# Performance work log

Measured on AMD Instinct MI355X. Metric: run time of the kernel, lower is better.

The kernel has to match this reference:

```python
import jax, jax.numpy as jnp
import numpy as np
from jax import lax

B, C, H, W = 4, 64, 128, 128
G, K, RED = 16, 7, 4        # groups, kernel size, reduce ratio
CR = C // RED               # reduced channels for kernel generation
EPS = 1e-5                  # BatchNorm eps (torch default)
DN = ('NCHW', 'OIHW', 'NCHW')


def setup_inputs() -> dict:
    key = jax.random.key(0)
    ks = jax.random.split(key, 5)
    return {
        'input': jax.random.normal(ks[0], (B, C, H, W), jnp.float32),
        # initial_mapping: depthwise 3x3 conv + pointwise 1x1 conv (bias=False)
        'w_dw': jax.random.normal(ks[1], (C, 1, 3, 3), jnp.float32) * 0.1,
        'w_pw': jax.random.normal(ks[2], (C, C), jnp.float32) * (1.0 / np.sqrt(C)),
        # sigma_mapping BatchNorm affine params
        'bn_gamma': jnp.ones((CR,), jnp.float32),
        'bn_beta': jnp.zeros((CR,), jnp.float32),
        # reduce / span 1x1 convs (bias=False)
        'w_reduce': jax.random.normal(ks[3], (CR, C), jnp.float32) * (1.0 / np.sqrt(C)),
        'w_span': jax.random.normal(ks[4], (K * K * G, CR), jnp.float32) * (1.0 / np.sqrt(CR)),
    }


def reference(input, w_dw, w_pw, bn_gamma, bn_beta, w_reduce, w_span):
    x = input
    # initial mapping: depthwise 3x3 (pad 1) then 1x1 pointwise
    h = lax.conv_general_dilated(x, w_dw, (1, 1), [(1, 1), (1, 1)],
                                 feature_group_count=C, dimension_numbers=DN)
    h = jnp.einsum('bchw,oc->bohw', h, w_pw)
    # unfold -> [B, C*K*K, H, W] with channel-major feature ordering (matches torch Unfold)
    patches = lax.conv_general_dilated_patches(h, (K, K), (1, 1), [(3, 3), (3, 3)],
                                               dimension_numbers=DN)
    patches = patches.reshape(B, G, C // G, K * K, H, W)
    # kernel generation: o_mapping is identity (stride 1 avg pool), then reduce -> BN(train) -> ReLU -> span
    r = jnp.einsum('bchw,oc->bohw', x, w_reduce)           # [B, CR, H, W]
    mean = r.mean(axis=(0, 2, 3), keepdims=True)
    var = r.var(axis=(0, 2, 3), keepdims=True)             # biased var, as torch BN training
    r = (r - mean) * lax.rsqrt(var + EPS) * bn_gamma[None, :, None, None] + bn_beta[None, :, None, None]
    r = jax.nn.relu(r)
    kern = jnp.einsum('bchw,oc->bohw', r, w_span)          # [B, G*K*K, H, W]
    kern = kern.reshape(B, G, 1, K * K, H, W)
    out = (kern * patches).sum(axis=3)                     # [B, G, C//G, H, W]
    return out.reshape(B, C, H, W)
```

## Files before the change

### kernel.cpp

```cpp
#include <hip/hip_runtime.h>

typedef _Float16 half2v __attribute__((ext_vector_type(2)));
typedef _Float16 half4v __attribute__((ext_vector_type(4)));
typedef _Float16 half8v __attribute__((ext_vector_type(8)));
typedef float f32x4 __attribute__((ext_vector_type(4)));

__launch_bounds__(256, 4)
__global__ void k_front(const float* __restrict__ in, const float* __restrict__ wdw,
                        const float* __restrict__ wpw, const float* __restrict__ wred,
                        _Float16* __restrict__ h16, _Float16* __restrict__ r16,
                        float* __restrict__ partial){
  __shared__ float4 s_in4[4][10][12];
  __shared__ __attribute__((aligned(16))) _Float16 s_dwh[64][72];
  __shared__ __attribute__((aligned(16))) _Float16 s_cvh[64][72];
  __shared__ float s_red[4][32];
  int t = threadIdx.x;
  int w = t >> 6, lane = t & 63;
  int lx = lane & 7, ly = lane >> 3;
  int c15 = lane & 15, hi = lane >> 4;
  int blk0 = blockIdx.x;

  int blk = ((blk0 & 7) << 7) | (blk0 >> 3);
  int tile = blk & 255, b = blk >> 8;
  int x0 = (tile & 15) << 3, y0 = (tile >> 4) << 3;
  const float* inb = in + ((long)b << 20) + ((long)(w << 2) << 14);

  const float* ap = wpw + (((w << 4) + c15) << 6) + (hi << 3);
  float4 ap0 = *(const float4*)(ap);
  float4 ap1 = *(const float4*)(ap + 4);
  float4 ap2 = *(const float4*)(ap + 32);
  float4 ap3 = *(const float4*)(ap + 36);
  const float* arp = wred + (c15 << 6) + (hi << 3);
  float4 ar0 = *(const float4*)(arp);
  float4 ar1 = *(const float4*)(arp + 4);
  float4 ar2 = *(const float4*)(arp + 32);
  float4 ar3 = *(const float4*)(arp + 36);
  half8v a_pw0 = {(_Float16)ap0.x,(_Float16)ap0.y,(_Float16)ap0.z,(_Float16)ap0.w,
                  (_Float16)ap1.x,(_Float16)ap1.y,(_Float16)ap1.z,(_Float16)ap1.w};
  half8v a_pw1 = {(_Float16)ap2.x,(_Float16)ap2.y,(_Float16)ap2.z,(_Float16)ap2.w,
                  (_Float16)ap3.x,(_Float16)ap3.y,(_Float16)ap3.z,(_Float16)ap3.w};
  half8v a_rd0 = {(_Float16)ar0.x,(_Float16)ar0.y,(_Float16)ar0.z,(_Float16)ar0.w,
                  (_Float16)ar1.x,(_Float16)ar1.y,(_Float16)ar1.z,(_Float16)ar1.w};
  half8v a_rd1 = {(_Float16)ar2.x,(_Float16)ar2.y,(_Float16)ar2.z,(_Float16)ar2.w,
                  (_Float16)ar3.x,(_Float16)ar3.y,(_Float16)ar3.z,(_Float16)ar3.w};

  int p1 = lane + 64;
  int ry0 = lane / 10, rx0 = lane - ry0 * 10;
  int ry1 = p1 / 10,   rx1 = p1 - ry1 * 10;
  int yy0 = y0 + ry0 - 1, xx0 = x0 + rx0 - 1;
  int yy1 = y0 + ry1 - 1, xx1 = x0 + rx1 - 1;
  bool ok0 = (unsigned)yy0 < 128u && (unsigned)xx0 < 128u;
  bool ok1 = (p1 < 100) && ((unsigned)yy1 < 128u) && ((unsigned)xx1 < 128u);
  int o0 = (yy0 << 7) + xx0, o1 = (yy1 << 7) + xx1;

  auto dw_dep = [&](int q){
    int wdbase = __builtin_amdgcn_readfirstlane(((q << 4) + (w << 2)) * 9);
    const float* wd = wdw + wdbase;
    float4 a = make_float4(0.f,0.f,0.f,0.f);
    float4 cv = make_float4(0.f,0.f,0.f,0.f);
    #pragma unroll
    for (int dy = 0; dy < 3; dy++){
      #pragma unroll
      for (int dx = 0; dx < 3; dx++){
        float4 v = s_in4[w][ly + dy][lx + dx];
        int k = dy * 3 + dx;
        a.x += v.x * wd[k];
        a.y += v.y * wd[9 + k];
        a.z += v.z * wd[18 + k];
        a.w += v.w * wd[27 + k];
        if (k == 4) cv = v;
      }
    }
    int cb = (q << 4) + (w << 2);
    half4v ah = {(_Float16)a.x,(_Float16)a.y,(_Float16)a.z,(_Float16)a.w};
    half4v eh = {(_Float16)cv.x,(_Float16)cv.y,(_Float16)cv.z,(_Float16)cv.w};
    *(half4v*)&s_dwh[lane][cb] = ah;
    *(half4v*)&s_cvh[lane][cb] = eh;
  };

  float4 vA0 = make_float4(0.f,0.f,0.f,0.f), vA1 = vA0, vB0 = vA0, vB1 = vA0;
  if (ok0){ vA0.x = inb[o0]; vA0.y = inb[o0+16384]; vA0.z = inb[o0+32768]; vA0.w = inb[o0+49152]; }
  if (ok1){ vA1.x = inb[o1]; vA1.y = inb[o1+16384]; vA1.z = inb[o1+32768]; vA1.w = inb[o1+49152]; }
  {
    const float* p1q = inb + (1L << 18);
    if (ok0){ vB0.x = p1q[o0]; vB0.y = p1q[o0+16384]; vB0.z = p1q[o0+32768]; vB0.w = p1q[o0+49152]; }
    if (ok1){ vB1.x = p1q[o1]; vB1.y = p1q[o1+16384]; vB1.z = p1q[o1+32768]; vB1.w = p1q[o1+49152]; }
  }

  #pragma unroll
  for (int qq = 0; qq < 2; qq++){
    s_in4[w][ry0][rx0] = vA0;
    if (p1 < 100) s_in4[w][ry1][rx1] = vA1;
    __builtin_amdgcn_wave_barrier();
    if (qq == 0){
      const float* pq = inb + (2L << 18);
      vA0 = make_float4(0.f,0.f,0.f,0.f); vA1 = vA0;
      if (ok0){ vA0.x = pq[o0]; vA0.y = pq[o0+16384]; vA0.z = pq[o0+32768]; vA0.w = pq[o0+49152]; }
      if (ok1){ vA1.x = pq[o1]; vA1.y = pq[o1+16384]; vA1.z = pq[o1+32768]; vA1.w = pq[o1+49152]; }
    }
    dw_dep(qq << 1);
    __builtin_amdgcn_wave_barrier();

    s_in4[w][ry0][rx0] = vB0;
    if (p1 < 100) s_in4[w][ry1][rx1] = vB1;
    __builtin_amdgcn_wave_barrier();
    if (qq == 0){
      const float* pq = inb + (3L << 18);
      vB0 = make_float4(0.f,0.f,0.f,0.f); vB1 = vB0;
      if (ok0){ vB0.x = pq[o0]; vB0.y = pq[o0+16384]; vB0.z = pq[o0+32768]; vB0.w = pq[o0+49152]; }
      if (ok1){ vB1.x = pq[o1]; vB1.y = pq[o1+16384]; vB1.z = pq[o1+32768]; vB1.w = pq[o1+49152]; }
    }
    dw_dep((qq << 1) + 1);
    __builtin_amdgcn_wave_barrier();
  }

  __syncthreads();

  f32x4 z = {0.f,0.f,0.f,0.f};
  f32x4 acc[4] = {z, z, z, z};
  #pragma unroll
  for (int tt = 0; tt < 4; tt++){
    half8v b0 = *(const half8v*)&s_dwh[(tt << 4) + c15][hi << 3];
    half8v b1 = *(const half8v*)&s_dwh[(tt << 4) + c15][32 + (hi << 3)];
    acc[tt] = __builtin_amdgcn_mfma_f32_16x16x32_f16(a_pw0, b0, acc[tt], 0, 0, 0);
    acc[tt] = __builtin_amdgcn_mfma_f32_16x16x32_f16(a_pw1, b1, acc[tt], 0, 0, 0);
  }
  #pragma unroll
  for (int tt = 0; tt < 4; tt++){
    int px = (tt << 4) + c15;
    int pyl = px >> 3, pxl = px & 7;
    int gout = (w << 2) + hi;
    long off = ((((long)((b << 4) + gout)) << 14) + ((y0 + pyl) << 7) + x0 + pxl) << 2;
    half4v hv = {(_Float16)acc[tt][0], (_Float16)acc[tt][1],
                 (_Float16)acc[tt][2], (_Float16)acc[tt][3]};
    *(half4v*)&h16[off] = hv;
  }

  f32x4 rac = z;
  {
    half8v b0 = *(const half8v*)&s_cvh[(w << 4) + c15][hi << 3];
    half8v b1 = *(const half8v*)&s_cvh[(w << 4) + c15][32 + (hi << 3)];
    rac = __builtin_amdgcn_mfma_f32_16x16x32_f16(a_rd0, b0, rac, 0, 0, 0);
    rac = __builtin_amdgcn_mfma_f32_16x16x32_f16(a_rd1, b1, rac, 0, 0, 0);
  }
  {
    int px = (w << 4) + c15;
    int pyl = px >> 3, pxl = px & 7;
    long roff = ((((long)b << 14) + ((y0 + pyl) << 7) + x0 + pxl) << 4) + (hi << 2);
    half4v rv4 = {(_Float16)rac[0], (_Float16)rac[1], (_Float16)rac[2], (_Float16)rac[3]};
    *(half4v*)&r16[roff] = rv4;
  }

  #pragma unroll
  for (int rr = 0; rr < 4; rr++){
    float v = rac[rr], s2 = v * v;
    #pragma unroll
    for (int m = 1; m < 16; m <<= 1){
      v  += __shfl_xor(v,  m, 64);
      s2 += __shfl_xor(s2, m, 64);
    }
    if (c15 == 0){
      int ch = (hi << 2) + rr;
      s_red[w][2 * ch]     = v;
      s_red[w][2 * ch + 1] = s2;
    }
  }
  __syncthreads();
  if (t < 32)
    partial[(blk0 << 5) + t] = s_red[0][t] + s_red[1][t] + s_red[2][t] + s_red[3][t];
}

__global__ void k_red(const float* __restrict__ partial, const float* __restrict__ gamma,
                      const float* __restrict__ beta, float* __restrict__ sb,
                      const float* __restrict__ wspan, _Float16* __restrict__ w16){
  __shared__ float sp[1024];
  int t = threadIdx.x;
  int c = t & 31, grp = t >> 5;
  float s = 0.f;
  #pragma unroll 4
  for (int i = grp; i < 1024; i += 32) s += partial[(i << 5) + c];
  sp[t] = s;
  for (int i = t; i < 12544; i += 1024) w16[i] = (_Float16)wspan[i];
  __syncthreads();
  if (t < 32){
    float v = 0.f;
    #pragma unroll
    for (int k = 0; k < 32; k++) v += sp[(k << 5) + t];
    sp[t] = v;
  }
  __syncthreads();
  if (t < 16){
    const float inv_n = 1.52587890625e-5f;
    float mean = sp[2 * t] * inv_n;
    float var  = sp[2 * t + 1] * inv_n - mean * mean;
    float inv  = rsqrtf(var + 1e-5f);
    float sc   = gamma[t] * inv;
    sb[2 * t]     = sc;
    sb[2 * t + 1] = beta[t] - mean * sc;
  }
}

__launch_bounds__(256)
__global__ void k_main(const _Float16* __restrict__ h16, const _Float16* __restrict__ r16,
                       const float* __restrict__ sb, const _Float16* __restrict__ w16,
                       float* __restrict__ out){
  __shared__ float4 s_h4[22][24];
  __shared__ float  s_sb[32];
  int t = threadIdx.x;
  int g = blockIdx.y, b = blockIdx.z;
  int bx = blockIdx.x;
  bx = ((bx & 7) << 3) | (bx >> 3);
  int tx0 = (bx & 7) << 4, ty0 = (bx >> 3) << 4;

  int ltx = t & 15, lty = t >> 4;
  int px = tx0 + ltx, py = ty0 + lty;

  const _Float16* rp = r16 + ((((long)b << 14) + (py << 7) + px) << 4);
  half8v ra = *(const half8v*)rp;
  half8v rb = *(const half8v*)(rp + 8);

  const _Float16* hp = h16 + (((long)((b << 4) + g)) << 16);
  for (int p = t; p < 484; p += 256){
    int ry = p / 22, rx = p - ry * 22;
    int yy = ty0 + ry - 3, xx = tx0 + rx - 3;
    float4 v = make_float4(0.f,0.f,0.f,0.f);
    if ((unsigned)yy < 128u && (unsigned)xx < 128u){
      half4v hh = *(const half4v*)&hp[(long)(((yy << 7) + xx) << 2)];
      v = make_float4((float)hh[0], (float)hh[1], (float)hh[2], (float)hh[3]);
    }
    s_h4[ry][rx] = v;
  }
  if (t < 32) s_sb[t] = sb[t];
  __syncthreads();

  float rv[16];
  #pragma unroll
  for (int c = 0; c < 8; c++){
    rv[c]     = fmaxf((float)ra[c] * s_sb[2*c]     + s_sb[2*c+1],     0.f);
    rv[c + 8] = fmaxf((float)rb[c] * s_sb[2*(c+8)] + s_sb[2*(c+8)+1], 0.f);
  }
#if __has_builtin(__builtin_amdgcn_fdot2)
  half2v rv2[8];
  #pragma unroll
  for (int j = 0; j < 8; j++){
    half2v pk; pk[0] = (_Float16)rv[2*j]; pk[1] = (_Float16)rv[2*j+1];
    rv2[j] = pk;
  }
#endif

  const _Float16* wg = w16 + g * 784;
#if __has_builtin(__builtin_amdgcn_fdot2)
  const half2v* wg2 = (const half2v*)wg;
#endif
  float acc0 = 0.f, acc1 = 0.f, acc2 = 0.f, acc3 = 0.f;
  #pragma unroll
  for (int kh = 0; kh < 7; kh++){
    #pragma unroll
    for (int kw = 0; kw < 7; kw++){
      int k = kh * 7 + kw;
      float kv0 = 0.f, kv1 = 0.f;
#if __has_builtin(__builtin_amdgcn_fdot2)
      #pragma unroll
      for (int j = 0; j < 4; j++){
        kv0 = __builtin_amdgcn_fdot2(rv2[j],     wg2[k*8 + j],     kv0, false);
        kv1 = __builtin_amdgcn_fdot2(rv2[j + 4], wg2[k*8 + j + 4], kv1, false);
      }
#else
      #pragma unroll
      for (int c = 0; c < 8; c++){
        kv0 += rv[c]     * (float)wg[k*16 + c];
        kv1 += rv[c + 8] * (float)wg[k*16 + c + 8];
      }
#endif
      float kv = kv0 + kv1;
      float4 hv = s_h4[lty + kh][ltx + kw];
      acc0 += kv * hv.x;
      acc1 += kv * hv.y;
      acc2 += kv * hv.z;
      acc3 += kv * hv.w;
    }
  }

  long obase = (((long)((b << 6) + (g << 2))) << 14) + (py << 7) + px;
  out[obase]         = acc0;
  out[obase + 16384] = acc1;
  out[obase + 32768] = acc2;
  out[obase + 49152] = acc3;
}

extern "C" void kernel_launch(void* const* d_in, const int* in_sizes, int n_in,
                              void* d_out, int out_size, void* d_ws, size_t ws_size,
                              hipStream_t stream){
  const float* in       = (const float*)d_in[0];
  const float* w_dw     = (const float*)d_in[1];
  const float* w_pw     = (const float*)d_in[2];
  const float* gamma    = (const float*)d_in[3];
  const float* beta     = (const float*)d_in[4];
  const float* w_reduce = (const float*)d_in[5];
  const float* w_span   = (const float*)d_in[6];
  float* out = (float*)d_out;

  _Float16* h16 = (_Float16*)d_ws;
  _Float16* r16 = h16 + 4194304;
  _Float16* w16 = r16 + 1048576;
  float* partial = (float*)(w16 + 16384);
  float* sb      = partial + 32768;

  k_front<<<1024, 256, 0, stream>>>(in, w_dw, w_pw, w_reduce, h16, r16, partial);
  k_red  <<<1, 1024, 0, stream>>>(partial, gamma, beta, sb, w_span, w16);
  dim3 grid(64, 16, 4);
  k_main <<<grid, 256, 0, stream>>>(h16, r16, sb, w16, out);
}
```

Measured before the change: 122.8 us.

## Compute two horizontal pixels per thread in k_main, sharing weights and halo rows

Each k_main thread now handles two adjacent pixels, so the tile widens to 32x16 and the grid halves. The per-tap weight loads are shared across both pixels, and each kh iteration loads one 8-wide row of the shared-memory halo into registers that both pixels reuse. Stores become float2 writes. The aim is to cut redundant weight and shared-memory loads and the halo overhead per pixel. In exchange it raises register pressure, leaves the kh loop rolled (unroll 1), and launches fewer blocks.

```diff
diff --git a/kernel.cpp b/kernel.cpp
--- a/kernel.cpp
+++ b/kernel.cpp
@@ -204,24 +204,25 @@
 __global__ void k_main(const _Float16* __restrict__ h16, const _Float16* __restrict__ r16,
                        const float* __restrict__ sb, const _Float16* __restrict__ w16,
                        float* __restrict__ out){
-  __shared__ float4 s_h4[22][24];
+  __shared__ float4 s_h4[22][38];
   __shared__ float  s_sb[32];
   int t = threadIdx.x;
   int g = blockIdx.y, b = blockIdx.z;
   int bx = blockIdx.x;
-  bx = ((bx & 7) << 3) | (bx >> 3);
-  int tx0 = (bx & 7) << 4, ty0 = (bx >> 3) << 4;
-
+  bx = ((bx & 7) << 2) | (bx >> 3);
+  int tx0 = (bx & 3) << 5, ty0 = (bx >> 2) << 4;
   int ltx = t & 15, lty = t >> 4;
-  int px = tx0 + ltx, py = ty0 + lty;
-
-  const _Float16* rp = r16 + ((((long)b << 14) + (py << 7) + px) << 4);
-  half8v ra = *(const half8v*)rp;
-  half8v rb = *(const half8v*)(rp + 8);
+  int pxA = tx0 + (ltx << 1), py = ty0 + lty;
+
+  const _Float16* rp = r16 + ((((long)b << 14) + (py << 7) + pxA) << 4);
+  half8v raA = *(const half8v*)rp;
+  half8v rbA = *(const half8v*)(rp + 8);
+  half8v raB = *(const half8v*)(rp + 16);
+  half8v rbB = *(const half8v*)(rp + 24);
 
   const _Float16* hp = h16 + (((long)((b << 4) + g)) << 16);
-  for (int p = t; p < 484; p += 256){
-    int ry = p / 22, rx = p - ry * 22;
+  for (int p = t; p < 836; p += 256){
+    int ry = p / 38, rx = p - ry * 38;
     int yy = ty0 + ry - 3, xx = tx0 + rx - 3;
     float4 v = make_float4(0.f,0.f,0.f,0.f);
     if ((unsigned)yy < 128u && (unsigned)xx < 128u){
@@ -233,59 +234,79 @@
   if (t < 32) s_sb[t] = sb[t];
   __syncthreads();
 
-  float rv[16];
-  #pragma unroll
-  for (int c = 0; c < 8; c++){
-    rv[c]     = fmaxf((float)ra[c] * s_sb[2*c]     + s_sb[2*c+1],     0.f);
-    rv[c + 8] = fmaxf((float)rb[c] * s_sb[2*(c+8)] + s_sb[2*(c+8)+1], 0.f);
-  }
-#if __has_builtin(__builtin_amdgcn_fdot2)
-  half2v rv2[8];
-  #pragma unroll
-  for (int j = 0; j < 8; j++){
-    half2v pk; pk[0] = (_Float16)rv[2*j]; pk[1] = (_Float16)rv[2*j+1];
-    rv2[j] = pk;
-  }
-#endif
+  half2v rvA[8], rvB[8];
+  {
+    float rv[16];
+    #pragma unroll
+    for (int c = 0; c < 8; c++){
+      rv[c]     = fmaxf((float)raA[c] * s_sb[2*c]     + s_sb[2*c+1],     0.f);
+      rv[c + 8] = fmaxf((float)rbA[c] * s_sb[2*(c+8)] + s_sb[2*(c+8)+1], 0.f);
+    }
+    #pragma unroll
+    for (int j = 0; j < 8; j++){
+      half2v pk; pk[0] = (_Float16)rv[2*j]; pk[1] = (_Float16)rv[2*j+1];
+      rvA[j] = pk;
+    }
+    #pragma unroll
+    for (int c = 0; c < 8; c++){
+      rv[c]     = fmaxf((float)raB[c] * s_sb[2*c]     + s_sb[2*c+1],     0.f);
+      rv[c + 8] = fmaxf((float)rbB[c] * s_sb[2*(c+8)] + s_sb[2*(c+8)+1], 0.f);
+    }
+    #pragma unroll
+    for (int j = 0; j < 8; j++){
+      half2v pk; pk[0] = (_Float16)rv[2*j]; pk[1] = (_Float16)rv[2*j+1];
+      rvB[j] = pk;
+    }
+  }
 
   const _Float16* wg = w16 + g * 784;
-#if __has_builtin(__builtin_amdgcn_fdot2)
   const half2v* wg2 = (const half2v*)wg;
-#endif
-  float acc0 = 0.f, acc1 = 0.f, acc2 = 0.f, acc3 = 0.f;
-  #pragma unroll
+
+  float aA0 = 0.f, aA1 = 0.f, aA2 = 0.f, aA3 = 0.f;
+  float aB0 = 0.f, aB1 = 0.f, aB2 = 0.f, aB3 = 0.f;
+
+  #pragma unroll 1
   for (int kh = 0; kh < 7; kh++){
+    float4 row[8];
+    #pragma unroll
+    for (int j = 0; j < 8; j++) row[j] = s_h4[lty + kh][(ltx << 1) + j];
     #pragma unroll
     for (int kw = 0; kw < 7; kw++){
       int k = kh * 7 + kw;
-      float kv0 = 0.f, kv1 = 0.f;
+      float kvA0 = 0.f, kvA1 = 0.f, kvB0 = 0.f, kvB1 = 0.f;
 #if __has_builtin(__builtin_amdgcn_fdot2)
       #pragma unroll
       for (int j = 0; j < 4; j++){
-        kv0 = __builtin_amdgcn_fdot2(rv2[j],     wg2[k*8 + j],     kv0, false);
-        kv1 = __builtin_amdgcn_fdot2(rv2[j + 4], wg2[k*8 + j + 4], kv1, false);
+        half2v w0 = wg2[k*8 + j], w1 = wg2[k*8 + j + 4];
+        kvA0 = __builtin_amdgcn_fdot2(rvA[j],     w0, kvA0, false);
+        kvA1 = __builtin_amdgcn_fdot2(rvA[j + 4], w1, kvA1, false);
+        kvB0 = __builtin_amdgcn_fdot2(rvB[j],     w0, kvB0, false);
+        kvB1 = __builtin_amdgcn_fdot2(rvB[j + 4], w1, kvB1, false);
       }
 #else
       #pragma unroll
-      for (int c = 0; c < 8; c++){
-        kv0 += rv[c]     * (float)wg[k*16 + c];
-        kv1 += rv[c + 8] * (float)wg[k*16 + c + 8];
+      for (int j = 0; j < 4; j++){
+        half2v w0 = wg2[k*8 + j], w1 = wg2[k*8 + j + 4];
+        kvA0 += (float)rvA[j][0]*(float)w0[0]   + (float)rvA[j][1]*(float)w0[1];
+        kvA1 += (float)rvA[j+4][0]*(float)w1[0] + (float)rvA[j+4][1]*(float)w1[1];
+        kvB0 += (float)rvB[j][0]*(float)w0[0]   + (float)rvB[j][1]*(float)w0[1];
+        kvB1 += (float)rvB[j+4][0]*(float)w1[0] + (float)rvB[j+4][1]*(float)w1[1];
       }
 #endif
-      float kv = kv0 + kv1;
-      float4 hv = s_h4[lty + kh][ltx + kw];
-      acc0 += kv * hv.x;
-      acc1 += kv * hv.y;
-      acc2 += kv * hv.z;
-      acc3 += kv * hv.w;
-    }
-  }
-
-  long obase = (((long)((b << 6) + (g << 2))) << 14) + (py << 7) + px;
-  out[obase]         = acc0;
-  out[obase + 16384] = acc1;
-  out[obase + 32768] = acc2;
-  out[obase + 49152] = acc3;
+      float kvA = kvA0 + kvA1, kvB = kvB0 + kvB1;
+      float4 hA = row[kw], hB = row[kw + 1];
+      aA0 += kvA * hA.x;  aB0 += kvB * hB.x;
+      aA1 += kvA * hA.y;  aB1 += kvB * hB.y;
+      aA2 += kvA * hA.z;  aB2 += kvB * hB.z;
+      aA3 += kvA * hA.w;  aB3 += kvB * hB.w;
+    }
+  }
+
+  long obase = (((long)((b << 6) + (g << 2))) << 14) + (py << 7) + pxA;
+  *(float2*)&out[obase]         = make_float2(aA0, aB0);
+  *(float2*)&out[obase + 16384] = make_float2(aA1, aB1);
+  *(float2*)&out[obase + 32768] = make_float2(aA2, aB2);
+  *(float2*)&out[obase + 49152] = make_float2(aA3, aB3);
 }
 
 extern "C" void kernel_launch(void* const* d_in, const int* in_sizes, int n_in,
@@ -308,6 +329,6 @@
 
   k_front<<<1024, 256, 0, stream>>>(in, w_dw, w_pw, w_reduce, h16, r16, partial);
   k_red  <<<1, 1024, 0, stream>>>(partial, gamma, beta, sb, w_span, w16);
-  dim3 grid(64, 16, 4);
+  dim3 grid(32, 16, 4);
   k_main <<<grid, 256, 0, stream>>>(h16, r16, sb, w16, out);
 }
```

New measurement: 125.0 us. No clear change (+1.8%).

## Fuse BN statistic reduction into front kernel via last-block ticket

Applied to the files above, without the earlier changes.

Removes the separate single-block k_red launch. Each front block converts a slice of w_span to fp16 and atomically increments a ticket, and the last block to finish reduces all partial sums and writes the BN scale and bias. This saves a kernel launch and the serialized single-block reduction gap. In exchange it adds a memset launch per call, a threadfence and atomic in every block, and a tail where one 256-thread block does the final reduction.

```diff
diff --git a/kernel.cpp b/kernel.cpp
--- a/kernel.cpp
+++ b/kernel.cpp
@@ -8,17 +8,26 @@
 __launch_bounds__(256, 4)
 __global__ void k_front(const float* __restrict__ in, const float* __restrict__ wdw,
                         const float* __restrict__ wpw, const float* __restrict__ wred,
+                        const float* __restrict__ wspan, const float* __restrict__ gamma,
+                        const float* __restrict__ beta,
                         _Float16* __restrict__ h16, _Float16* __restrict__ r16,
-                        float* __restrict__ partial){
+                        float* __restrict__ partial, float* __restrict__ sb,
+                        unsigned int* __restrict__ ticket, _Float16* __restrict__ w16){
   __shared__ float4 s_in4[4][10][12];
   __shared__ __attribute__((aligned(16))) _Float16 s_dwh[64][72];
   __shared__ __attribute__((aligned(16))) _Float16 s_cvh[64][72];
   __shared__ float s_red[4][32];
+  __shared__ int s_last;
   int t = threadIdx.x;
   int w = t >> 6, lane = t & 63;
   int lx = lane & 7, ly = lane >> 3;
   int c15 = lane & 15, hi = lane >> 4;
   int blk0 = blockIdx.x;
+
+  {
+    int i = blk0 * 256 + t;
+    if (i < 12544) w16[i] = (_Float16)wspan[i];
+  }
 
   int blk = ((blk0 & 7) << 7) | (blk0 >> 3);
   int tile = blk & 255, b = blk >> 8;
@@ -168,35 +177,38 @@
   __syncthreads();
   if (t < 32)
     partial[(blk0 << 5) + t] = s_red[0][t] + s_red[1][t] + s_red[2][t] + s_red[3][t];
-}
-
-__global__ void k_red(const float* __restrict__ partial, const float* __restrict__ gamma,
-                      const float* __restrict__ beta, float* __restrict__ sb,
-                      const float* __restrict__ wspan, _Float16* __restrict__ w16){
-  __shared__ float sp[1024];
-  int t = threadIdx.x;
-  int c = t & 31, grp = t >> 5;
-  float s = 0.f;
-  #pragma unroll 4
-  for (int i = grp; i < 1024; i += 32) s += partial[(i << 5) + c];
-  sp[t] = s;
-  for (int i = t; i < 12544; i += 1024) w16[i] = (_Float16)wspan[i];
+
+  __threadfence();
+  if (t == 0){
+    unsigned int old = atomicAdd(ticket, 1u);
+    s_last = (old == 1023u);
+  }
   __syncthreads();
-  if (t < 32){
-    float v = 0.f;
-    #pragma unroll
-    for (int k = 0; k < 32; k++) v += sp[(k << 5) + t];
-    sp[t] = v;
-  }
-  __syncthreads();
-  if (t < 16){
-    const float inv_n = 1.52587890625e-5f;
-    float mean = sp[2 * t] * inv_n;
-    float var  = sp[2 * t + 1] * inv_n - mean * mean;
-    float inv  = rsqrtf(var + 1e-5f);
-    float sc   = gamma[t] * inv;
-    sb[2 * t]     = sc;
-    sb[2 * t + 1] = beta[t] - mean * sc;
+  if (s_last){
+    float* sc = (float*)s_cvh;
+    int c = t & 31;
+    float s = 0.f;
+    for (int i = t >> 5; i < 1024; i += 8)
+      s += __hip_atomic_load(&partial[(i << 5) + c], __ATOMIC_RELAXED,
+                             __HIP_MEMORY_SCOPE_AGENT);
+    sc[t] = s;
+    __syncthreads();
+    if (t < 32){
+      float v = 0.f;
+      #pragma unroll
+      for (int k2 = 0; k2 < 8; k2++) v += sc[(k2 << 5) + t];
+      sc[256 + t] = v;
+    }
+    __syncthreads();
+    if (t < 16){
+      const float inv_n = 1.52587890625e-5f;
+      float mean = sc[256 + 2 * t] * inv_n;
+      float var  = sc[256 + 2 * t + 1] * inv_n - mean * mean;
+      float inv  = rsqrtf(var + 1e-5f);
+      float scl  = gamma[t] * inv;
+      sb[2 * t]     = scl;
+      sb[2 * t + 1] = beta[t] - mean * scl;
+    }
   }
 }
 
@@ -305,9 +317,11 @@
   _Float16* w16 = r16 + 1048576;
   float* partial = (float*)(w16 + 16384);
   float* sb      = partial + 32768;
-
-  k_front<<<1024, 256, 0, stream>>>(in, w_dw, w_pw, w_reduce, h16, r16, partial);
-  k_red  <<<1, 1024, 0, stream>>>(partial, gamma, beta, sb, w_span, w16);
+  unsigned int* ticket = (unsigned int*)(sb + 32);
+
+  hipMemsetAsync(ticket, 0, sizeof(unsigned int), stream);
+  k_front<<<1024, 256, 0, stream>>>(in, w_dw, w_pw, w_reduce, w_span, gamma, beta,
+                                    h16, r16, partial, sb, ticket, w16);
   dim3 grid(64, 16, 4);
   k_main <<<grid, 256, 0, stream>>>(h16, r16, sb, w16, out);
 }
```

New measurement: 250.8 us. 104% more time.
